# Kernel optimization log

Hardware: AMD Instinct MI355X
Metric: run time of the kernel (lower is better)

Reference implementation:

```python
import jax, jax.numpy as jnp
import numpy as np

H, T, D = 16, 4096, 64   # heads, total packed tokens, head_dim
NSEQ = 8                 # packed variable-length sequences

def setup_inputs() -> dict:
    key = jax.random.key(0)
    k1, k2, k3 = jax.random.split(key, 3)
    q = jax.random.normal(k1, (1, H, T, D), dtype=jnp.float32)
    k = jax.random.normal(k2, (1, H, T, D), dtype=jnp.float32)
    v = jax.random.normal(k3, (1, H, T, D), dtype=jnp.float32)
    # cu_seqlens: prefix sums of per-sequence lengths (equal 512-token segments here)
    cu_seqlens = jnp.arange(NSEQ + 1, dtype=jnp.int32) * (T // NSEQ)
    return {"q": q, "k": k, "v": v, "cu_seqlens": cu_seqlens,
            "block_q_len": 128, "block_k_len": 512}

def reference(q, k, v, cu_seqlens, block_q_len, block_k_len):
    # Faithful to source: scale = 1.0 / d**(-0.5) == sqrt(d)
    d = q.shape[-1]
    scale = 1.0 / d ** (-0.5)
    # [1,H,T,D] -> [T,H,D] packed layout (transpose(1,2).squeeze(0))
    qp = jnp.swapaxes(q, 1, 2)[0]
    kp = jnp.swapaxes(k, 1, 2)[0]
    vp = jnp.swapaxes(v, 1, 2)[0]
    t = qp.shape[0]
    # segment id of each packed token from cu_seqlens
    seg = jnp.searchsorted(cu_seqlens[1:], jnp.arange(t), side="right")
    # tokens attend only within their own sequence (causal=False, dropout=0)
    mask = seg[:, None] == seg[None, :]                      # [T,T]
    scores = jnp.einsum("qhd,khd->hqk", qp, kp) * scale      # [H,T,T]
    scores = jnp.where(mask[None, :, :], scores, -jnp.inf)
    p = jax.nn.softmax(scores, axis=-1)
    out = jnp.einsum("hqk,khd->qhd", p, vp)                  # [T,H,D]
    return out
```

## Files before the change

### kernel.cpp

```cpp
#include <hip/hip_runtime.h>
#include <stdint.h>

typedef short  bf16x8 __attribute__((ext_vector_type(8)));
typedef float  f32x4  __attribute__((ext_vector_type(4)));
typedef unsigned short u16;
typedef u16    u16x4  __attribute__((ext_vector_type(4)));

#define HD 16
#define DD 64
#define BQ 64
#define BK 64

__device__ __forceinline__ u16 f2bf(float f) {
  uint32_t u = __float_as_uint(f);
  u = (u + 0x7FFFu + ((u >> 16) & 1u)) >> 16;
  return (u16)u;
}

__device__ __forceinline__ bf16x8 ldsw8(const u16* base, int row, int col) {
  int idx = (row * 64 + col) ^ ((row & 7) << 3);
  return *reinterpret_cast<const bf16x8*>(base + idx);
}
__device__ __forceinline__ bf16x8 ldsv8(const u16* base, int d, int col) {
  int idx = (d * 64 + col) ^ ((((d >> 2) ^ d) & 7) << 3);
  return *reinterpret_cast<const bf16x8*>(base + idx);
}

__global__ __launch_bounds__(256) void fa_fwd(
    const float* __restrict__ q, const float* __restrict__ k,
    const float* __restrict__ v, const int* __restrict__ cu,
    float* __restrict__ out, int T, int nseq, int nqt)
{
  __shared__ __align__(16) u16 sKhi[BK * DD];
  __shared__ __align__(16) u16 sKlo[BK * DD];
  __shared__ __align__(16) u16 sVt [DD * BK];
  __shared__ __align__(16) u16 sP  [4][16 * BK];

  const int nwg = nqt * HD;
  const int x8 = blockIdx.x & 7, mm = blockIdx.x >> 3;
  const int q8 = nwg >> 3, r8 = nwg & 7;
  const int wid = (x8 < r8 ? x8 * (q8 + 1) : r8 * (q8 + 1) + (x8 - r8) * q8) + mm;
  const int h    = wid / nqt;
  const int tile = wid - h * nqt;

  int seg = -1, row0 = 0, sbeg = 0, send = 0;
  {
    int acc = 0;
    for (int s = 0; s < nseq; ++s) {
      int b = cu[s], e = cu[s + 1];
      int nt = (e - b + BQ - 1) >> 6;
      if (seg < 0 && tile < acc + nt) {
        seg = s;
        int local = tile - acc;
        row0 = b + local * BQ; sbeg = b; send = e;
      }
      acc += nt;
    }
  }
  if (seg < 0) return;
  const int rows = min(BQ, send - row0);

  const int tid  = threadIdx.x;
  const int wv   = tid >> 6;
  const int lane = tid & 63;
  const int g    = lane >> 4;
  const int c    = lane & 15;

  const float SC = 8.0f * 1.4426950408889634f;
  bf16x8 qhi[2], qlo[2];
  {
    const int qrl = min(wv * 16 + c, rows - 1);
    const float* qp = q + ((size_t)h * T + (row0 + qrl)) * DD;
    #pragma unroll
    for (int w = 0; w < 2; ++w) {
      int d0 = w * 32 + g * 8;
      float4 a = *reinterpret_cast<const float4*>(qp + d0);
      float4 b = *reinterpret_cast<const float4*>(qp + d0 + 4);
      float f[8] = {a.x, a.y, a.z, a.w, b.x, b.y, b.z, b.w};
      #pragma unroll
      for (int i = 0; i < 8; ++i) {
        float s  = f[i] * SC;
        u16   hb = f2bf(s);
        float hf = __uint_as_float(((uint32_t)hb) << 16);
        qhi[w][i] = (short)hb;
        qlo[w][i] = (short)f2bf(s - hf);
      }
    }
  }

  const int kd0  = (tid & 15) * 4;
  const int kkey = tid >> 4;
  const int vdg  = tid & 15;
  const int vkb  = tid >> 4;

  f32x4 zero4 = {0.f, 0.f, 0.f, 0.f};
  f32x4 oacc[4];
  #pragma unroll
  for (int dt = 0; dt < 4; ++dt) oacc[dt] = zero4;
  float mrun[4], lrun[4];
  #pragma unroll
  for (int j = 0; j < 4; ++j) { mrun[j] = -1e30f; lrun[j] = 0.f; }

  const int nt = (send - sbeg + BK - 1) >> 6;

  for (int t = 0; t < nt; ++t) {
    const int kt0 = sbeg + t * BK;
    __syncthreads();

    {
      #pragma unroll
      for (int p = 0; p < 4; ++p) {
        int key = p * 16 + kkey;
        int gk  = kt0 + key; gk = gk < send ? gk : send - 1;
        float4 kv = *reinterpret_cast<const float4*>(k + ((size_t)h * T + gk) * DD + kd0);
        float f[4] = {kv.x, kv.y, kv.z, kv.w};
        u16x4 hi4, lo4;
        #pragma unroll
        for (int i = 0; i < 4; ++i) {
          u16   hb = f2bf(f[i]);
          float hf = __uint_as_float(((uint32_t)hb) << 16);
          hi4[i] = hb;
          lo4[i] = f2bf(f[i] - hf);
        }
        int idx = (key * 64 + kd0) ^ ((key & 7) << 3);
        *reinterpret_cast<u16x4*>(sKhi + idx) = hi4;
        *reinterpret_cast<u16x4*>(sKlo + idx) = lo4;
      }
      #pragma unroll
      for (int it = 0; it < 2; ++it) {
        int kp = it * 16 + vkb;
        int g0 = kt0 + 2 * kp;     g0 = g0 < send ? g0 : send - 1;
        int g1 = kt0 + 2 * kp + 1; g1 = g1 < send ? g1 : send - 1;
        float4 va = *reinterpret_cast<const float4*>(v + ((size_t)h * T + g0) * DD + 4 * vdg);
        float4 vb = *reinterpret_cast<const float4*>(v + ((size_t)h * T + g1) * DD + 4 * vdg);
        float a[4] = {va.x, va.y, va.z, va.w};
        float b[4] = {vb.x, vb.y, vb.z, vb.w};
        #pragma unroll
        for (int i = 0; i < 4; ++i) {
          int d   = 4 * vdg + i;
          int idx = (d * 64 + 2 * kp) ^ ((((d >> 2) ^ d) & 7) << 3);
          *reinterpret_cast<uint32_t*>(sVt + idx) =
              (uint32_t)f2bf(a[i]) | ((uint32_t)f2bf(b[i]) << 16);
        }
      }
    }
    __syncthreads();

    f32x4 sacc[4];
    #pragma unroll
    for (int kt = 0; kt < 4; ++kt) sacc[kt] = zero4;
    #pragma unroll
    for (int kt = 0; kt < 4; ++kt) {
      int krow = kt * 16 + c;
      bf16x8 kh0 = ldsw8(sKhi, krow,      g * 8);
      bf16x8 kh1 = ldsw8(sKhi, krow, 32 + g * 8);
      bf16x8 kl0 = ldsw8(sKlo, krow,      g * 8);
      bf16x8 kl1 = ldsw8(sKlo, krow, 32 + g * 8);
      sacc[kt] = __builtin_amdgcn_mfma_f32_16x16x32_bf16(qhi[0], kh0, sacc[kt], 0, 0, 0);
      sacc[kt] = __builtin_amdgcn_mfma_f32_16x16x32_bf16(qhi[1], kh1, sacc[kt], 0, 0, 0);
      sacc[kt] = __builtin_amdgcn_mfma_f32_16x16x32_bf16(qlo[0], kh0, sacc[kt], 0, 0, 0);
      sacc[kt] = __builtin_amdgcn_mfma_f32_16x16x32_bf16(qlo[1], kh1, sacc[kt], 0, 0, 0);
      sacc[kt] = __builtin_amdgcn_mfma_f32_16x16x32_bf16(qhi[0], kl0, sacc[kt], 0, 0, 0);
      sacc[kt] = __builtin_amdgcn_mfma_f32_16x16x32_bf16(qhi[1], kl1, sacc[kt], 0, 0, 0);
    }

    if (kt0 + BK > send) {
      #pragma unroll
      for (int kt = 0; kt < 4; ++kt) {
        int gk = kt0 + kt * 16 + c;
        if (gk >= send) {
          sacc[kt][0] = -3.0e38f; sacc[kt][1] = -3.0e38f;
          sacc[kt][2] = -3.0e38f; sacc[kt][3] = -3.0e38f;
        }
      }
    }

    float mrow[4];
    #pragma unroll
    for (int j = 0; j < 4; ++j)
      mrow[j] = fmaxf(fmaxf(sacc[0][j], sacc[1][j]), fmaxf(sacc[2][j], sacc[3][j]));
    #pragma unroll
    for (int off = 1; off < 16; off <<= 1)
      #pragma unroll
      for (int j = 0; j < 4; ++j)
        mrow[j] = fmaxf(mrow[j], __shfl_xor(mrow[j], off, 64));

    float alpha[4];
    #pragma unroll
    for (int j = 0; j < 4; ++j) {
      float mn = fmaxf(mrun[j], mrow[j]);
      alpha[j] = exp2f(mrun[j] - mn);
      mrun[j] = mn;
    }

    float lrow[4] = {0.f, 0.f, 0.f, 0.f};
    u16* pb = sP[wv];
    #pragma unroll
    for (int kt = 0; kt < 4; ++kt) {
      int key = kt * 16 + c;
      #pragma unroll
      for (int j = 0; j < 4; ++j) {
        float pv = exp2f(sacc[kt][j] - mrun[j]);
        lrow[j] += pv;
        int row = g * 4 + j;
        pb[(row * 64 + key) ^ ((row & 7) << 3)] = f2bf(pv);
      }
    }
    #pragma unroll
    for (int off = 1; off < 16; off <<= 1)
      #pragma unroll
      for (int j = 0; j < 4; ++j)
        lrow[j] += __shfl_xor(lrow[j], off, 64);
    #pragma unroll
    for (int j = 0; j < 4; ++j) lrun[j] = lrun[j] * alpha[j] + lrow[j];
    #pragma unroll
    for (int dt = 0; dt < 4; ++dt)
      #pragma unroll
      for (int j = 0; j < 4; ++j) oacc[dt][j] *= alpha[j];

    bf16x8 pf0 = ldsw8(pb, c,      g * 8);
    bf16x8 pf1 = ldsw8(pb, c, 32 + g * 8);
    #pragma unroll
    for (int dt = 0; dt < 4; ++dt) {
      bf16x8 v0 = ldsv8(sVt, dt * 16 + c,      g * 8);
      bf16x8 v1 = ldsv8(sVt, dt * 16 + c, 32 + g * 8);
      oacc[dt] = __builtin_amdgcn_mfma_f32_16x16x32_bf16(pf0, v0, oacc[dt], 0, 0, 0);
      oacc[dt] = __builtin_amdgcn_mfma_f32_16x16x32_bf16(pf1, v1, oacc[dt], 0, 0, 0);
    }
  }

  float inv[4];
  #pragma unroll
  for (int j = 0; j < 4; ++j) inv[j] = 1.0f / lrun[j];
  #pragma unroll
  for (int dt = 0; dt < 4; ++dt) {
    #pragma unroll
    for (int j = 0; j < 4; ++j) {
      int rl = wv * 16 + g * 4 + j;
      if (rl < rows)
        out[((size_t)(row0 + rl) * HD + h) * DD + dt * 16 + c] = oacc[dt][j] * inv[j];
    }
  }
}

extern "C" void kernel_launch(void* const* d_in, const int* in_sizes, int n_in,
                              void* d_out, int out_size, void* d_ws, size_t ws_size,
                              hipStream_t stream) {
  const float* q  = (const float*)d_in[0];
  const float* k  = (const float*)d_in[1];
  const float* v  = (const float*)d_in[2];
  const int*   cu = (const int*)d_in[3];
  int nseq = in_sizes[3] - 1;
  int T    = in_sizes[0] / (HD * DD);
  int nqt  = T / BQ + nseq;
  int nwg  = nqt * HD;
  fa_fwd<<<dim3(nwg), dim3(256), 0, stream>>>(q, k, v, cu, (float*)d_out, T, nseq, nqt);
}
```

Baseline: 136.2 us.

## Double query rows per workgroup and use packed bf16 conversion intrinsics

Raises the query tile from 64 to 128 rows, so each wave now handles two 16-row groups against the same K/V tile held in shared memory. Each K/V load and its bf16 split conversion is therefore shared by twice as many queries, which halves global K/V traffic and conversion work. The custom rounding helper is replaced with HIP bf16 intrinsics, including packed two-value conversions. The trade-offs are half as many workgroups (fewer in flight across the GPU) and higher register pressure from the doubled accumulators and Q fragments.

```diff
diff --git a/kernel.cpp b/kernel.cpp
--- a/kernel.cpp
+++ b/kernel.cpp
@@ -1,20 +1,23 @@
 #include <hip/hip_runtime.h>
+#include <hip/hip_bf16.h>
 #include <stdint.h>
 
 typedef short  bf16x8 __attribute__((ext_vector_type(8)));
 typedef float  f32x4  __attribute__((ext_vector_type(4)));
 typedef unsigned short u16;
-typedef u16    u16x4  __attribute__((ext_vector_type(4)));
 
 #define HD 16
 #define DD 64
-#define BQ 64
+#define BQ 128
 #define BK 64
 
-__device__ __forceinline__ u16 f2bf(float f) {
-  uint32_t u = __float_as_uint(f);
-  u = (u + 0x7FFFu + ((u >> 16) & 1u)) >> 16;
-  return (u16)u;
+__device__ __forceinline__ u16 bf1(float a) {
+  __hip_bfloat16 h = __float2bfloat16(a);
+  union { __hip_bfloat16 h; u16 u; } cv; cv.h = h; return cv.u;
+}
+__device__ __forceinline__ uint32_t pk2(float a, float b) {
+  __hip_bfloat162 h = __float22bfloat162_rn(make_float2(a, b));
+  union { __hip_bfloat162 h; uint32_t u; } cv; cv.h = h; return cv.u;
 }
 
 __device__ __forceinline__ bf16x8 ldsw8(const u16* base, int row, int col) {
@@ -48,7 +51,7 @@
     int acc = 0;
     for (int s = 0; s < nseq; ++s) {
       int b = cu[s], e = cu[s + 1];
-      int nt = (e - b + BQ - 1) >> 6;
+      int nt = (e - b + BQ - 1) >> 7;
       if (seg < 0 && tile < acc + nt) {
         seg = s;
         int local = tile - acc;
@@ -67,9 +70,10 @@
   const int c    = lane & 15;
 
   const float SC = 8.0f * 1.4426950408889634f;
-  bf16x8 qhi[2], qlo[2];
-  {
-    const int qrl = min(wv * 16 + c, rows - 1);
+  bf16x8 qhi[2][2], qlo[2][2];
+  #pragma unroll
+  for (int u = 0; u < 2; ++u) {
+    const int qrl = min(u * 64 + wv * 16 + c, rows - 1);
     const float* qp = q + ((size_t)h * T + (row0 + qrl)) * DD;
     #pragma unroll
     for (int w = 0; w < 2; ++w) {
@@ -80,10 +84,10 @@
       #pragma unroll
       for (int i = 0; i < 8; ++i) {
         float s  = f[i] * SC;
-        u16   hb = f2bf(s);
+        u16   hb = bf1(s);
         float hf = __uint_as_float(((uint32_t)hb) << 16);
-        qhi[w][i] = (short)hb;
-        qlo[w][i] = (short)f2bf(s - hf);
+        qhi[u][w][i] = (short)hb;
+        qlo[u][w][i] = (short)bf1(s - hf);
       }
     }
   }
@@ -94,12 +98,15 @@
   const int vkb  = tid >> 4;
 
   f32x4 zero4 = {0.f, 0.f, 0.f, 0.f};
-  f32x4 oacc[4];
+  f32x4 oacc[2][4];
+  float mrun[2][4], lrun[2][4];
   #pragma unroll
-  for (int dt = 0; dt < 4; ++dt) oacc[dt] = zero4;
-  float mrun[4], lrun[4];
-  #pragma unroll
-  for (int j = 0; j < 4; ++j) { mrun[j] = -1e30f; lrun[j] = 0.f; }
+  for (int u = 0; u < 2; ++u) {
+    #pragma unroll
+    for (int dt = 0; dt < 4; ++dt) oacc[u][dt] = zero4;
+    #pragma unroll
+    for (int j = 0; j < 4; ++j) { mrun[u][j] = -1e30f; lrun[u][j] = 0.f; }
+  }
 
   const int nt = (send - sbeg + BK - 1) >> 6;
 
@@ -113,18 +120,16 @@
         int key = p * 16 + kkey;
         int gk  = kt0 + key; gk = gk < send ? gk : send - 1;
         float4 kv = *reinterpret_cast<const float4*>(k + ((size_t)h * T + gk) * DD + kd0);
-        float f[4] = {kv.x, kv.y, kv.z, kv.w};
-        u16x4 hi4, lo4;
-        #pragma unroll
-        for (int i = 0; i < 4; ++i) {
-          u16   hb = f2bf(f[i]);
-          float hf = __uint_as_float(((uint32_t)hb) << 16);
-          hi4[i] = hb;
-          lo4[i] = f2bf(f[i] - hf);
-        }
+        uint32_t h01 = pk2(kv.x, kv.y), h23 = pk2(kv.z, kv.w);
+        float hf0 = __uint_as_float(h01 << 16);
+        float hf1 = __uint_as_float(h01 & 0xffff0000u);
+        float hf2 = __uint_as_float(h23 << 16);
+        float hf3 = __uint_as_float(h23 & 0xffff0000u);
+        uint32_t l01 = pk2(kv.x - hf0, kv.y - hf1), l23 = pk2(kv.z - hf2, kv.w - hf3);
         int idx = (key * 64 + kd0) ^ ((key & 7) << 3);
-        *reinterpret_cast<u16x4*>(sKhi + idx) = hi4;
-        *reinterpret_cast<u16x4*>(sKlo + idx) = lo4;
+        uint2 hh = {h01, h23}, ll = {l01, l23};
+        *reinterpret_cast<uint2*>(sKhi + idx) = hh;
+        *reinterpret_cast<uint2*>(sKlo + idx) = ll;
       }
       #pragma unroll
       for (int it = 0; it < 2; ++it) {
@@ -139,106 +144,111 @@
         for (int i = 0; i < 4; ++i) {
           int d   = 4 * vdg + i;
           int idx = (d * 64 + 2 * kp) ^ ((((d >> 2) ^ d) & 7) << 3);
-          *reinterpret_cast<uint32_t*>(sVt + idx) =
-              (uint32_t)f2bf(a[i]) | ((uint32_t)f2bf(b[i]) << 16);
+          *reinterpret_cast<uint32_t*>(sVt + idx) = pk2(a[i], b[i]);
         }
       }
     }
     __syncthreads();
 
-    f32x4 sacc[4];
-    #pragma unroll
-    for (int kt = 0; kt < 4; ++kt) sacc[kt] = zero4;
-    #pragma unroll
-    for (int kt = 0; kt < 4; ++kt) {
-      int krow = kt * 16 + c;
-      bf16x8 kh0 = ldsw8(sKhi, krow,      g * 8);
-      bf16x8 kh1 = ldsw8(sKhi, krow, 32 + g * 8);
-      bf16x8 kl0 = ldsw8(sKlo, krow,      g * 8);
-      bf16x8 kl1 = ldsw8(sKlo, krow, 32 + g * 8);
-      sacc[kt] = __builtin_amdgcn_mfma_f32_16x16x32_bf16(qhi[0], kh0, sacc[kt], 0, 0, 0);
-      sacc[kt] = __builtin_amdgcn_mfma_f32_16x16x32_bf16(qhi[1], kh1, sacc[kt], 0, 0, 0);
-      sacc[kt] = __builtin_amdgcn_mfma_f32_16x16x32_bf16(qlo[0], kh0, sacc[kt], 0, 0, 0);
-      sacc[kt] = __builtin_amdgcn_mfma_f32_16x16x32_bf16(qlo[1], kh1, sacc[kt], 0, 0, 0);
-      sacc[kt] = __builtin_amdgcn_mfma_f32_16x16x32_bf16(qhi[0], kl0, sacc[kt], 0, 0, 0);
-      sacc[kt] = __builtin_amdgcn_mfma_f32_16x16x32_bf16(qhi[1], kl1, sacc[kt], 0, 0, 0);
-    }
-
-    if (kt0 + BK > send) {
+    #pragma unroll
+    for (int u = 0; u < 2; ++u) {
+      f32x4 sacc[4];
+      #pragma unroll
+      for (int kt = 0; kt < 4; ++kt) sacc[kt] = zero4;
       #pragma unroll
       for (int kt = 0; kt < 4; ++kt) {
-        int gk = kt0 + kt * 16 + c;
-        if (gk >= send) {
-          sacc[kt][0] = -3.0e38f; sacc[kt][1] = -3.0e38f;
-          sacc[kt][2] = -3.0e38f; sacc[kt][3] = -3.0e38f;
+        int krow = kt * 16 + c;
+        bf16x8 kh0 = ldsw8(sKhi, krow,      g * 8);
+        bf16x8 kh1 = ldsw8(sKhi, krow, 32 + g * 8);
+        bf16x8 kl0 = ldsw8(sKlo, krow,      g * 8);
+        bf16x8 kl1 = ldsw8(sKlo, krow, 32 + g * 8);
+        sacc[kt] = __builtin_amdgcn_mfma_f32_16x16x32_bf16(qhi[u][0], kh0, sacc[kt], 0, 0, 0);
+        sacc[kt] = __builtin_amdgcn_mfma_f32_16x16x32_bf16(qhi[u][1], kh1, sacc[kt], 0, 0, 0);
+        sacc[kt] = __builtin_amdgcn_mfma_f32_16x16x32_bf16(qlo[u][0], kh0, sacc[kt], 0, 0, 0);
+        sacc[kt] = __builtin_amdgcn_mfma_f32_16x16x32_bf16(qlo[u][1], kh1, sacc[kt], 0, 0, 0);
+        sacc[kt] = __builtin_amdgcn_mfma_f32_16x16x32_bf16(qhi[u][0], kl0, sacc[kt], 0, 0, 0);
+        sacc[kt] = __builtin_amdgcn_mfma_f32_16x16x32_bf16(qhi[u][1], kl1, sacc[kt], 0, 0, 0);
+      }
+
+      if (kt0 + BK > send) {
+        #pragma unroll
+        for (int kt = 0; kt < 4; ++kt) {
+          int gk = kt0 + kt * 16 + c;
+          if (gk >= send) {
+            sacc[kt][0] = -3.0e38f; sacc[kt][1] = -3.0e38f;
+            sacc[kt][2] = -3.0e38f; sacc[kt][3] = -3.0e38f;
+          }
         }
       }
-    }
-
-    float mrow[4];
-    #pragma unroll
-    for (int j = 0; j < 4; ++j)
-      mrow[j] = fmaxf(fmaxf(sacc[0][j], sacc[1][j]), fmaxf(sacc[2][j], sacc[3][j]));
-    #pragma unroll
-    for (int off = 1; off < 16; off <<= 1)
+
+      float mrow[4];
       #pragma unroll
       for (int j = 0; j < 4; ++j)
-        mrow[j] = fmaxf(mrow[j], __shfl_xor(mrow[j], off, 64));
-
-    float alpha[4];
-    #pragma unroll
-    for (int j = 0; j < 4; ++j) {
-      float mn = fmaxf(mrun[j], mrow[j]);
-      alpha[j] = exp2f(mrun[j] - mn);
-      mrun[j] = mn;
-    }
-
-    float lrow[4] = {0.f, 0.f, 0.f, 0.f};
-    u16* pb = sP[wv];
-    #pragma unroll
-    for (int kt = 0; kt < 4; ++kt) {
-      int key = kt * 16 + c;
+        mrow[j] = fmaxf(fmaxf(sacc[0][j], sacc[1][j]), fmaxf(sacc[2][j], sacc[3][j]));
+      #pragma unroll
+      for (int off = 1; off < 16; off <<= 1)
+        #pragma unroll
+        for (int j = 0; j < 4; ++j)
+          mrow[j] = fmaxf(mrow[j], __shfl_xor(mrow[j], off, 64));
+
+      float alpha[4];
       #pragma unroll
       for (int j = 0; j < 4; ++j) {
-        float pv = exp2f(sacc[kt][j] - mrun[j]);
-        lrow[j] += pv;
-        int row = g * 4 + j;
-        pb[(row * 64 + key) ^ ((row & 7) << 3)] = f2bf(pv);
-      }
-    }
-    #pragma unroll
-    for (int off = 1; off < 16; off <<= 1)
-      #pragma unroll
-      for (int j = 0; j < 4; ++j)
-        lrow[j] += __shfl_xor(lrow[j], off, 64);
-    #pragma unroll
-    for (int j = 0; j < 4; ++j) lrun[j] = lrun[j] * alpha[j] + lrow[j];
-    #pragma unroll
-    for (int dt = 0; dt < 4; ++dt)
-      #pragma unroll
-      for (int j = 0; j < 4; ++j) oacc[dt][j] *= alpha[j];
-
-    bf16x8 pf0 = ldsw8(pb, c,      g * 8);
-    bf16x8 pf1 = ldsw8(pb, c, 32 + g * 8);
+        float mn = fmaxf(mrun[u][j], mrow[j]);
+        alpha[j] = exp2f(mrun[u][j] - mn);
+        mrun[u][j] = mn;
+      }
+
+      float lrow[4] = {0.f, 0.f, 0.f, 0.f};
+      u16* pb = sP[wv];
+      #pragma unroll
+      for (int kt = 0; kt < 4; ++kt) {
+        int key = kt * 16 + c;
+        #pragma unroll
+        for (int j = 0; j < 4; ++j) {
+          float pv = exp2f(sacc[kt][j] - mrun[u][j]);
+          lrow[j] += pv;
+          int row = g * 4 + j;
+          pb[(row * 64 + key) ^ ((row & 7) << 3)] = bf1(pv);
+        }
+      }
+      #pragma unroll
+      for (int off = 1; off < 16; off <<= 1)
+        #pragma unroll
+        for (int j = 0; j < 4; ++j)
+          lrow[j] += __shfl_xor(lrow[j], off, 64);
+      #pragma unroll
+      for (int j = 0; j < 4; ++j) lrun[u][j] = lrun[u][j] * alpha[j] + lrow[j];
+      #pragma unroll
+      for (int dt = 0; dt < 4; ++dt)
+        #pragma unroll
+        for (int j = 0; j < 4; ++j) oacc[u][dt][j] *= alpha[j];
+
+      bf16x8 pf0 = ldsw8(pb, c,      g * 8);
+      bf16x8 pf1 = ldsw8(pb, c, 32 + g * 8);
+      #pragma unroll
+      for (int dt = 0; dt < 4; ++dt) {
+        bf16x8 v0 = ldsv8(sVt, dt * 16 + c,      g * 8);
+        bf16x8 v1 = ldsv8(sVt, dt * 16 + c, 32 + g * 8);
+        oacc[u][dt] = __builtin_amdgcn_mfma_f32_16x16x32_bf16(pf0, v0, oacc[u][dt], 0, 0, 0);
+        oacc[u][dt] = __builtin_amdgcn_mfma_f32_16x16x32_bf16(pf1, v1, oacc[u][dt], 0, 0, 0);
+      }
+    }
+  }
+
+  #pragma unroll
+  for (int u = 0; u < 2; ++u) {
+    float inv[4];
+    #pragma unroll
+    for (int j = 0; j < 4; ++j) inv[j] = 1.0f / lrun[u][j];
     #pragma unroll
     for (int dt = 0; dt < 4; ++dt) {
-      bf16x8 v0 = ldsv8(sVt, dt * 16 + c,      g * 8);
-      bf16x8 v1 = ldsv8(sVt, dt * 16 + c, 32 + g * 8);
-      oacc[dt] = __builtin_amdgcn_mfma_f32_16x16x32_bf16(pf0, v0, oacc[dt], 0, 0, 0);
-      oacc[dt] = __builtin_amdgcn_mfma_f32_16x16x32_bf16(pf1, v1, oacc[dt], 0, 0, 0);
-    }
-  }
-
-  float inv[4];
-  #pragma unroll
-  for (int j = 0; j < 4; ++j) inv[j] = 1.0f / lrun[j];
-  #pragma unroll
-  for (int dt = 0; dt < 4; ++dt) {
-    #pragma unroll
-    for (int j = 0; j < 4; ++j) {
-      int rl = wv * 16 + g * 4 + j;
-      if (rl < rows)
-        out[((size_t)(row0 + rl) * HD + h) * DD + dt * 16 + c] = oacc[dt][j] * inv[j];
+      #pragma unroll
+      for (int j = 0; j < 4; ++j) {
+        int rl = u * 64 + wv * 16 + g * 4 + j;
+        if (rl < rows)
+          out[((size_t)(row0 + rl) * HD + h) * DD + dt * 16 + c] = oacc[u][dt][j] * inv[j];
+      }
     }
   }
 }
```

Result: faster. 131.2 us (-3.7%).

## Double query tile to 128 rows with 512 threads and use packed bf16 converts

Applied to the files above, without the earlier changes.

Each workgroup now covers 128 query rows with eight waves, so every K/V tile staged and split into bf16 hi/lo parts in shared memory serves twice as many queries, and per-thread staging work is halved. The manual bf16 rounding is replaced by HIP conversion intrinsics, including a packed two-float convert for K and V. The cost is half as many workgroups and more registers and shared memory per block, which may reduce occupancy.

```diff
diff --git a/kernel.cpp b/kernel.cpp
--- a/kernel.cpp
+++ b/kernel.cpp
@@ -1,20 +1,23 @@
 #include <hip/hip_runtime.h>
+#include <hip/hip_bf16.h>
 #include <stdint.h>
 
 typedef short  bf16x8 __attribute__((ext_vector_type(8)));
 typedef float  f32x4  __attribute__((ext_vector_type(4)));
 typedef unsigned short u16;
-typedef u16    u16x4  __attribute__((ext_vector_type(4)));
 
 #define HD 16
 #define DD 64
-#define BQ 64
+#define BQ 128
 #define BK 64
 
-__device__ __forceinline__ u16 f2bf(float f) {
-  uint32_t u = __float_as_uint(f);
-  u = (u + 0x7FFFu + ((u >> 16) & 1u)) >> 16;
-  return (u16)u;
+__device__ __forceinline__ u16 bf1(float a) {
+  __hip_bfloat16 h = __float2bfloat16(a);
+  union { __hip_bfloat16 h; u16 u; } cv; cv.h = h; return cv.u;
+}
+__device__ __forceinline__ uint32_t pk2(float a, float b) {
+  __hip_bfloat162 h = __float22bfloat162_rn(make_float2(a, b));
+  union { __hip_bfloat162 h; uint32_t u; } cv; cv.h = h; return cv.u;
 }
 
 __device__ __forceinline__ bf16x8 ldsw8(const u16* base, int row, int col) {
@@ -26,7 +29,7 @@
   return *reinterpret_cast<const bf16x8*>(base + idx);
 }
 
-__global__ __launch_bounds__(256) void fa_fwd(
+__global__ __launch_bounds__(512) void fa_fwd(
     const float* __restrict__ q, const float* __restrict__ k,
     const float* __restrict__ v, const int* __restrict__ cu,
     float* __restrict__ out, int T, int nseq, int nqt)
@@ -34,7 +37,7 @@
   __shared__ __align__(16) u16 sKhi[BK * DD];
   __shared__ __align__(16) u16 sKlo[BK * DD];
   __shared__ __align__(16) u16 sVt [DD * BK];
-  __shared__ __align__(16) u16 sP  [4][16 * BK];
+  __shared__ __align__(16) u16 sP  [8][16 * BK];
 
   const int nwg = nqt * HD;
   const int x8 = blockIdx.x & 7, mm = blockIdx.x >> 3;
@@ -48,7 +51,7 @@
     int acc = 0;
     for (int s = 0; s < nseq; ++s) {
       int b = cu[s], e = cu[s + 1];
-      int nt = (e - b + BQ - 1) >> 6;
+      int nt = (e - b + BQ - 1) >> 7;
       if (seg < 0 && tile < acc + nt) {
         seg = s;
         int local = tile - acc;
@@ -80,18 +83,18 @@
       #pragma unroll
       for (int i = 0; i < 8; ++i) {
         float s  = f[i] * SC;
-        u16   hb = f2bf(s);
+        u16   hb = bf1(s);
         float hf = __uint_as_float(((uint32_t)hb) << 16);
         qhi[w][i] = (short)hb;
-        qlo[w][i] = (short)f2bf(s - hf);
-      }
-    }
-  }
-
-  const int kd0  = (tid & 15) * 4;
-  const int kkey = tid >> 4;
-  const int vdg  = tid & 15;
-  const int vkb  = tid >> 4;
+        qlo[w][i] = (short)bf1(s - hf);
+      }
+    }
+  }
+
+  const int kd0   = (tid & 15) * 4;
+  const int kkey  = tid >> 4;
+  const int vdg   = tid & 15;
+  const int vkb   = tid >> 4;
 
   f32x4 zero4 = {0.f, 0.f, 0.f, 0.f};
   f32x4 oacc[4];
@@ -109,26 +112,23 @@
 
     {
       #pragma unroll
-      for (int p = 0; p < 4; ++p) {
-        int key = p * 16 + kkey;
+      for (int p = 0; p < 2; ++p) {
+        int key = p * 32 + kkey;
         int gk  = kt0 + key; gk = gk < send ? gk : send - 1;
         float4 kv = *reinterpret_cast<const float4*>(k + ((size_t)h * T + gk) * DD + kd0);
-        float f[4] = {kv.x, kv.y, kv.z, kv.w};
-        u16x4 hi4, lo4;
-        #pragma unroll
-        for (int i = 0; i < 4; ++i) {
-          u16   hb = f2bf(f[i]);
-          float hf = __uint_as_float(((uint32_t)hb) << 16);
-          hi4[i] = hb;
-          lo4[i] = f2bf(f[i] - hf);
-        }
+        uint32_t h01 = pk2(kv.x, kv.y), h23 = pk2(kv.z, kv.w);
+        float hf0 = __uint_as_float(h01 << 16);
+        float hf1 = __uint_as_float(h01 & 0xffff0000u);
+        float hf2 = __uint_as_float(h23 << 16);
+        float hf3 = __uint_as_float(h23 & 0xffff0000u);
+        uint32_t l01 = pk2(kv.x - hf0, kv.y - hf1), l23 = pk2(kv.z - hf2, kv.w - hf3);
         int idx = (key * 64 + kd0) ^ ((key & 7) << 3);
-        *reinterpret_cast<u16x4*>(sKhi + idx) = hi4;
-        *reinterpret_cast<u16x4*>(sKlo + idx) = lo4;
-      }
-      #pragma unroll
-      for (int it = 0; it < 2; ++it) {
-        int kp = it * 16 + vkb;
+        uint2 hh = {h01, h23}, ll = {l01, l23};
+        *reinterpret_cast<uint2*>(sKhi + idx) = hh;
+        *reinterpret_cast<uint2*>(sKlo + idx) = ll;
+      }
+      {
+        int kp = vkb;
         int g0 = kt0 + 2 * kp;     g0 = g0 < send ? g0 : send - 1;
         int g1 = kt0 + 2 * kp + 1; g1 = g1 < send ? g1 : send - 1;
         float4 va = *reinterpret_cast<const float4*>(v + ((size_t)h * T + g0) * DD + 4 * vdg);
@@ -139,8 +139,7 @@
         for (int i = 0; i < 4; ++i) {
           int d   = 4 * vdg + i;
           int idx = (d * 64 + 2 * kp) ^ ((((d >> 2) ^ d) & 7) << 3);
-          *reinterpret_cast<uint32_t*>(sVt + idx) =
-              (uint32_t)f2bf(a[i]) | ((uint32_t)f2bf(b[i]) << 16);
+          *reinterpret_cast<uint32_t*>(sVt + idx) = pk2(a[i], b[i]);
         }
       }
     }
@@ -203,7 +202,7 @@
         float pv = exp2f(sacc[kt][j] - mrun[j]);
         lrow[j] += pv;
         int row = g * 4 + j;
-        pb[(row * 64 + key) ^ ((row & 7) << 3)] = f2bf(pv);
+        pb[(row * 64 + key) ^ ((row & 7) << 3)] = bf1(pv);
       }
     }
     #pragma unroll
@@ -254,5 +253,5 @@
   int T    = in_sizes[0] / (HD * DD);
   int nqt  = T / BQ + nseq;
   int nwg  = nqt * HD;
-  fa_fwd<<<dim3(nwg), dim3(256), 0, stream>>>(q, k, v, cu, (float*)d_out, T, nseq, nqt);
-}
+  fa_fwd<<<dim3(nwg), dim3(512), 0, stream>>>(q, k, v, cu, (float*)d_out, T, nseq, nqt);
+}
```

Result: no change. 137.3 us (+0.8%).
